# Optimization experiments

Hardware: AMD Instinct MI355X
Metric: run time of the kernel (lower is better)

The kernel has to match this reference:

```python
import jax, jax.numpy as jnp
import numpy as np

N_NODES = 100000
N_EDGES = 1600000
HIDDEN = 256
CONV_OUT = 128
OUT = 2


def setup_inputs() -> dict:
    key = jax.random.key(0)
    k1, k2, k3, k4, k5, k6, k7 = jax.random.split(key, 7)
    x = jax.random.normal(k1, (N_NODES, HIDDEN), dtype=jnp.float32)
    edge_index = jax.random.randint(k2, (2, N_EDGES), 0, N_NODES, dtype=jnp.int64)
    edge_weight = jax.random.uniform(k3, (N_EDGES,), dtype=jnp.float32)
    # GCNConv parameters (lin: hidden->128, bias added after aggregation)
    W1 = jax.random.normal(k4, (HIDDEN, CONV_OUT), dtype=jnp.float32) / np.sqrt(HIDDEN)
    b1 = jnp.zeros((CONV_OUT,), dtype=jnp.float32)
    # head Linear(128, out_channels)
    W2 = jax.random.normal(k5, (CONV_OUT, OUT), dtype=jnp.float32) / np.sqrt(CONV_OUT)
    b2 = jax.random.normal(k6, (OUT,), dtype=jnp.float32) * 0.01
    return {"x": x, "edge_index": edge_index, "edge_weight": edge_weight,
            "W1": W1, "b1": b1, "W2": W2, "b2": b2}


def reference(x, edge_index, edge_weight, W1, b1, W2, b2):
    # GCNConv (use_weights=True branch, no relu), dropout in eval mode (identity), then Linear.
    N = x.shape[0]
    src, dst = edge_index[0], edge_index[1]
    # add self-loops with weight 1 (PyG default fill_value=1.0)
    loop = jnp.arange(N, dtype=src.dtype)
    src = jnp.concatenate([src, loop])
    dst = jnp.concatenate([dst, loop])
    w = jnp.concatenate([edge_weight, jnp.ones((N,), dtype=edge_weight.dtype)])
    # symmetric normalization: norm = d^{-1/2}[src] * w * d^{-1/2}[dst]
    deg = jax.ops.segment_sum(w, dst, num_segments=N)
    dinv = jnp.where(deg > 0, jax.lax.rsqrt(deg), 0.0)
    norm = dinv[src] * w * dinv[dst]
    # transform then gather-scatter aggregate
    h = x @ W1                                   # [N, 128]
    msgs = norm[:, None] * h[src]                # [E+N, 128]
    agg = jax.ops.segment_sum(msgs, dst, num_segments=N) + b1  # [N, 128]
    return agg @ W2 + b2                         # [N, out_channels]
```

## Files before the change

kernel.cpp:

```cpp
#include <hip/hip_runtime.h>

#define N_NODES 100000
#define N_EDGES 1600000
#define HIDDEN 256

#define BSH 7
#define BNODES 128
#define NB 782
#define NPB 256
#define EPB 6250
#define SLOTS 32
#define NZB 12500


__global__ __launch_bounds__(1024) void k_place(
        const int* __restrict__ ei, const float* __restrict__ ew,
        const float* __restrict__ W1, const float* __restrict__ b1,
        const float* __restrict__ W2, const float* __restrict__ b2,
        int* __restrict__ cnt, uint2* __restrict__ rec,
        float* __restrict__ W12, float* __restrict__ cvec) {
    const int tid = threadIdx.x, bid = blockIdx.x;
    if (bid == NPB) {
        if (tid < HIDDEN) {
            const float4* w1r = (const float4*)(W1 + (size_t)tid * 128);
            float a0 = 0.f, a1 = 0.f;
#pragma unroll 8
            for (int k4 = 0; k4 < 32; ++k4) {
                float4 v = w1r[k4];
                a0 += v.x * W2[8 * k4 + 0]; a1 += v.x * W2[8 * k4 + 1];
                a0 += v.y * W2[8 * k4 + 2]; a1 += v.y * W2[8 * k4 + 3];
                a0 += v.z * W2[8 * k4 + 4]; a1 += v.z * W2[8 * k4 + 5];
                a0 += v.w * W2[8 * k4 + 6]; a1 += v.w * W2[8 * k4 + 7];
            }
            W12[2 * tid] = a0; W12[2 * tid + 1] = a1;
            if (tid < 2) {
                float acc = b2[tid];
                for (int k = 0; k < 128; ++k) acc += b1[k] * W2[2 * k + tid];
                cvec[tid] = acc;
            }
        }
        return;
    }
    __shared__ int cursor[NB];
    for (int i = tid; i < NB; i += 1024) cursor[i] = 0;
    __syncthreads();
    const int e0 = bid * EPB, e1 = e0 + EPB;
    for (int e = e0 + tid; e < e1; e += 1024) {
        int d = ei[N_EDGES + e];
        int s = ei[e];
        float wv = ew[e];
        int bk = ((unsigned)d) >> BSH;
        int pos = atomicAdd(&cursor[bk], 1);
        if (pos < SLOTS)
            rec[((size_t)bk * NPB + bid) * SLOTS + pos] =
                make_uint2((unsigned)s | ((unsigned)(d & (BNODES - 1)) << 17),
                           __float_as_uint(wv));
    }
    __syncthreads();
    for (int i = tid; i < NB; i += 1024)
        cnt[(size_t)i * NPB + bid] = min(cursor[i], SLOTS);
}

__global__ __launch_bounds__(256) void k_zdeg(
        const float* __restrict__ x, const float* __restrict__ W12,
        const uint2* __restrict__ rec, const int* __restrict__ cnt,
        float* __restrict__ z, float* __restrict__ dinv) {
    __shared__ float acc[BNODES];
    const int tid = threadIdx.x, bid = blockIdx.x;
    if (bid < NB) {
        if (tid < BNODES) acc[tid] = 1.0f;
        __syncthreads();
        const int n = cnt[(size_t)bid * NPB + tid];
        const uint2* r = rec + ((size_t)bid * NPB + tid) * SLOTS;
        for (int i = 0; i < n; ++i) {
            uint2 q = r[i];
            atomicAdd(&acc[q.x >> 17], __uint_as_float(q.y));
        }
        __syncthreads();
        if (tid < BNODES) {
            int node = bid * BNODES + tid;
            if (node < N_NODES) dinv[node] = rsqrtf(acc[tid]);
        }
    } else {
        const int lane = tid & 63;
        const float2 w0 = ((const float2*)W12)[lane * 4 + 0];
        const float2 w1 = ((const float2*)W12)[lane * 4 + 1];
        const float2 w2 = ((const float2*)W12)[lane * 4 + 2];
        const float2 w3 = ((const float2*)W12)[lane * 4 + 3];
        const int n0 = (((bid - NB) * 4) + (tid >> 6)) * 2;
        const float4 xa = *(const float4*)(x + (size_t)n0 * HIDDEN + lane * 4);
        const float4 xb = *(const float4*)(x + (size_t)(n0 + 1) * HIDDEN + lane * 4);
        float a0 = xa.x * w0.x + xa.y * w1.x + xa.z * w2.x + xa.w * w3.x;
        float a1 = xa.x * w0.y + xa.y * w1.y + xa.z * w2.y + xa.w * w3.y;
        float c0 = xb.x * w0.x + xb.y * w1.x + xb.z * w2.x + xb.w * w3.x;
        float c1 = xb.x * w0.y + xb.y * w1.y + xb.z * w2.y + xb.w * w3.y;
#pragma unroll
        for (int m = 32; m >= 1; m >>= 1) {
            a0 += __shfl_xor(a0, m, 64);
            a1 += __shfl_xor(a1, m, 64);
            c0 += __shfl_xor(c0, m, 64);
            c1 += __shfl_xor(c1, m, 64);
        }
        if (lane == 0) *(float4*)(z + 2 * n0) = make_float4(a0, a1, c0, c1);
    }
}

__global__ __launch_bounds__(256) void k_gather(
        const uint2* __restrict__ rec, const int* __restrict__ cnt,
        const float* __restrict__ dinv, const float* __restrict__ z,
        const float* __restrict__ cvec, float2* __restrict__ out) {
    __shared__ float ax[BNODES], ay[BNODES];
    const int tid = threadIdx.x, b = blockIdx.x;
    if (tid < BNODES) { ax[tid] = 0.f; ay[tid] = 0.f; }
    __syncthreads();
    const int n = cnt[(size_t)b * NPB + tid];
    const uint2* r = rec + ((size_t)b * NPB + tid) * SLOTS;
    for (int i = 0; i < n; ++i) {
        uint2 q = r[i];
        int s = (int)(q.x & 0x1FFFFu);
        float nw = dinv[s] * __uint_as_float(q.y);
        float2 zv = ((const float2*)z)[s];
        int dl = (int)(q.x >> 17);
        atomicAdd(&ax[dl], nw * zv.x);
        atomicAdd(&ay[dl], nw * zv.y);
    }
    __syncthreads();
    if (tid < BNODES) {
        int node = b * BNODES + tid;
        if (node < N_NODES) {
            float di = dinv[node];
            float2 zv = ((const float2*)z)[node];
            out[node] = make_float2(di * ax[tid] + di * di * zv.x + cvec[0],
                                    di * ay[tid] + di * di * zv.y + cvec[1]);
        }
    }
}

extern "C" void kernel_launch(void* const* d_in, const int* in_sizes, int n_in,
                              void* d_out, int out_size, void* d_ws, size_t ws_size,
                              hipStream_t stream) {
    const float* x  = (const float*)d_in[0];
    const int*   ei = (const int*)d_in[1];
    const float* ew = (const float*)d_in[2];
    const float* W1 = (const float*)d_in[3];
    const float* b1 = (const float*)d_in[4];
    const float* W2 = (const float*)d_in[5];
    const float* b2 = (const float*)d_in[6];
    float2* out = (float2*)d_out;

    char* ws = (char*)d_ws;
    uint2*  rec  = (uint2*)ws;           size_t off = (size_t)NB * NPB * SLOTS * 8;
    int*    cnt  = (int*)(ws + off);     off += (size_t)NB * NPB * 4;
    float*  dinv = (float*)(ws + off);   off += (size_t)N_NODES * 4;
    float*  z    = (float*)(ws + off);   off += (size_t)N_NODES * 8;
    float*  W12  = (float*)(ws + off);   off += HIDDEN * 2 * 4;
    float*  cvec = (float*)(ws + off);   off += 16;

    k_place <<<NPB + 1, 1024, 0, stream>>>(ei, ew, W1, b1, W2, b2, cnt, rec, W12, cvec);
    k_zdeg  <<<NB + NZB, 256, 0, stream>>>(x, W12, rec, cnt, z, dinv);
    k_gather<<<NB, 256, 0, stream>>>(rec, cnt, dinv, z, cvec, out);
}
```

Baseline: 76.43 us.

## Use grid-stride nontemporal z projection and paired record loads in gathers

The z projection part of k_zdeg drops from 12500 single-shot blocks to 1024 grid-stride blocks that read x with nontemporal loads, which cuts block launch overhead and keeps the streamed x data out of cache. Both the degree loop and the gather loop now load two edge records at once as a uint4 and issue their dependent loads for two edges together, which adds memory-level parallelism. Fewer blocks could lower occupancy for the bandwidth-bound x read.

Result: slower. 78.09 us (+2.2%).

```diff
diff --git a/kernel.cpp b/kernel.cpp
--- a/kernel.cpp
+++ b/kernel.cpp
@@ -10,7 +10,10 @@
 #define NPB 256
 #define EPB 6250
 #define SLOTS 32
-#define NZB 12500
+#define NZB 1024
+#define NZW (NZB * 4)
+
+typedef float f32x4 __attribute__((ext_vector_type(4)));
 
 
 __global__ __launch_bounds__(1024) void k_place(
@@ -72,7 +75,13 @@
         __syncthreads();
         const int n = cnt[(size_t)bid * NPB + tid];
         const uint2* r = rec + ((size_t)bid * NPB + tid) * SLOTS;
-        for (int i = 0; i < n; ++i) {
+        int i = 0;
+        for (; i + 2 <= n; i += 2) {
+            uint4 q = *(const uint4*)(r + i);
+            atomicAdd(&acc[q.x >> 17], __uint_as_float(q.y));
+            atomicAdd(&acc[q.z >> 17], __uint_as_float(q.w));
+        }
+        if (i < n) {
             uint2 q = r[i];
             atomicAdd(&acc[q.x >> 17], __uint_as_float(q.y));
         }
@@ -87,21 +96,24 @@
         const float2 w1 = ((const float2*)W12)[lane * 4 + 1];
         const float2 w2 = ((const float2*)W12)[lane * 4 + 2];
         const float2 w3 = ((const float2*)W12)[lane * 4 + 3];
-        const int n0 = (((bid - NB) * 4) + (tid >> 6)) * 2;
-        const float4 xa = *(const float4*)(x + (size_t)n0 * HIDDEN + lane * 4);
-        const float4 xb = *(const float4*)(x + (size_t)(n0 + 1) * HIDDEN + lane * 4);
-        float a0 = xa.x * w0.x + xa.y * w1.x + xa.z * w2.x + xa.w * w3.x;
-        float a1 = xa.x * w0.y + xa.y * w1.y + xa.z * w2.y + xa.w * w3.y;
-        float c0 = xb.x * w0.x + xb.y * w1.x + xb.z * w2.x + xb.w * w3.x;
-        float c1 = xb.x * w0.y + xb.y * w1.y + xb.z * w2.y + xb.w * w3.y;
+        const int g = (bid - NB) * 4 + (tid >> 6);
+        for (int p = g; p < N_NODES / 2; p += NZW) {
+            const float* base = x + (size_t)(2 * p) * HIDDEN + lane * 4;
+            f32x4 xa = __builtin_nontemporal_load((const f32x4*)base);
+            f32x4 xb = __builtin_nontemporal_load((const f32x4*)(base + HIDDEN));
+            float a0 = xa.x * w0.x + xa.y * w1.x + xa.z * w2.x + xa.w * w3.x;
+            float a1 = xa.x * w0.y + xa.y * w1.y + xa.z * w2.y + xa.w * w3.y;
+            float c0 = xb.x * w0.x + xb.y * w1.x + xb.z * w2.x + xb.w * w3.x;
+            float c1 = xb.x * w0.y + xb.y * w1.y + xb.z * w2.y + xb.w * w3.y;
 #pragma unroll
-        for (int m = 32; m >= 1; m >>= 1) {
-            a0 += __shfl_xor(a0, m, 64);
-            a1 += __shfl_xor(a1, m, 64);
-            c0 += __shfl_xor(c0, m, 64);
-            c1 += __shfl_xor(c1, m, 64);
+            for (int m = 1; m <= 32; m <<= 1) {
+                a0 += __shfl_xor(a0, m, 64);
+                a1 += __shfl_xor(a1, m, 64);
+                c0 += __shfl_xor(c0, m, 64);
+                c1 += __shfl_xor(c1, m, 64);
+            }
+            if (lane == 0) *(float4*)(z + 4 * p) = make_float4(a0, a1, c0, c1);
         }
-        if (lane == 0) *(float4*)(z + 2 * n0) = make_float4(a0, a1, c0, c1);
     }
 }
 
@@ -115,7 +127,22 @@
     __syncthreads();
     const int n = cnt[(size_t)b * NPB + tid];
     const uint2* r = rec + ((size_t)b * NPB + tid) * SLOTS;
-    for (int i = 0; i < n; ++i) {
+    int i = 0;
+    for (; i + 2 <= n; i += 2) {
+        uint4 q = *(const uint4*)(r + i);
+        int s0 = (int)(q.x & 0x1FFFFu), s1 = (int)(q.z & 0x1FFFFu);
+        float di0 = dinv[s0], di1 = dinv[s1];
+        float2 z0 = ((const float2*)z)[s0];
+        float2 z1 = ((const float2*)z)[s1];
+        float nw0 = di0 * __uint_as_float(q.y);
+        float nw1 = di1 * __uint_as_float(q.w);
+        int d0 = (int)(q.x >> 17), d1 = (int)(q.z >> 17);
+        atomicAdd(&ax[d0], nw0 * z0.x);
+        atomicAdd(&ay[d0], nw0 * z0.y);
+        atomicAdd(&ax[d1], nw1 * z1.x);
+        atomicAdd(&ay[d1], nw1 * z1.y);
+    }
+    if (i < n) {
         uint2 q = r[i];
         int s = (int)(q.x & 0x1FFFFu);
         float nw = dinv[s] * __uint_as_float(q.y);
```
